# Kernel tuning notes

Measured on AMD Instinct MI355X. Metric: run time of the kernel, lower is better.

Reference implementation:

```python
import jax, jax.numpy as jnp
import numpy as np

TEMP = 0.1
EPS = 1e-12  # F.normalize eps


def setup_inputs() -> dict:
    key = jax.random.key(0)
    k1, k2 = jax.random.split(key)
    B, C, N = 8, 128, 4096
    features = jax.random.normal(k1, (B, C, N), dtype=jnp.float32)
    labels_all = jax.random.randint(k2, (B, N), 0, 16, dtype=jnp.int32)
    return {"features": features, "labels_all": labels_all}


def _per_cloud_loss(features_map, labels):
    # features_map: [C, N], labels: [N]
    v = features_map.T  # [N, C]
    v = v / jnp.maximum(jnp.linalg.norm(v, axis=1, keepdims=True), EPS)
    dp = jnp.exp(jnp.matmul(v, v.T) / TEMP)  # [N, N]
    n = dp.shape[0]
    # remove diagonal (dot_products - diag(diagonal))
    dp = dp * (1.0 - jnp.eye(n, dtype=dp.dtype))
    mask = labels[:, None] == labels[None, :]  # [N, N]
    positives = jnp.sum(jnp.where(mask, dp, 0.0), axis=1)
    negatives = jnp.sum(jnp.where(mask, 0.0, dp), axis=1)
    deviation = -jnp.log(positives / (positives + negatives))
    return jnp.mean(deviation)


def reference(features, labels_all):
    # features: [B, C, N], labels_all: [B, N]
    losses = jax.vmap(_per_cloud_loss)(features, labels_all)  # [B]
    return jnp.mean(losses)
```

## Files before the change

### kernel.cpp

```cpp
#include <hip/hip_runtime.h>
#include <hip/hip_bf16.h>
#include <math.h>

#define BATCH 8
#define NPTS 4096
#define CH 128
#define CTG 8
#define ROWS 128
#define CHUNK 32
#define NCHUNK (NPTS / (CTG * CHUNK))
#define NBUF 3

#define SQRT_TEMP_LOG2E 3.79828256f

typedef __attribute__((ext_vector_type(4))) float    f32x4;
typedef __attribute__((ext_vector_type(4))) int      i32x4;
typedef __attribute__((ext_vector_type(8))) short    bf16x8;
typedef __attribute__((ext_vector_type(4))) _Float16 f16x4;

typedef __attribute__((address_space(3))) unsigned int lds_uint;
typedef __attribute__((address_space(1))) const unsigned int gbl_uint;

__device__ __forceinline__ void load_lds16(const void* g, const void* l) {
    __builtin_amdgcn_global_load_lds((gbl_uint*)g, (lds_uint*)l, 16, 0, 0);
}

__device__ __forceinline__ float fast_exp2(float x) {
    return __builtin_amdgcn_exp2f(x);
}

__device__ __forceinline__ f32x4 mfma16(f16x4 a, f16x4 b, f32x4 c) {
#if __has_builtin(__builtin_amdgcn_mfma_f32_16x16x16f16)
    return __builtin_amdgcn_mfma_f32_16x16x16f16(a, b, c, 0, 0, 0);
#else
    f32x4 d = c;
    asm volatile("v_mfma_f32_16x16x16_f16 %0, %1, %2, %0"
                 : "+v"(d) : "v"(a), "v"(b));
    return d;
#endif
}

__global__ __launch_bounds__(256) void normalize_kernel(
    const float* __restrict__ f, __hip_bfloat16* __restrict__ vn,
    float* __restrict__ pos, float* __restrict__ neg, float* __restrict__ out)
{
    int idx = blockIdx.x * 256 + threadIdx.x;
    int point = idx >> 3, q = idx & 7;
    int b = point >> 12, n = point & (NPTS - 1);
    const float* base = f + (size_t)b * CH * NPTS + (size_t)(q * 16) * NPTS + n;

    float x[16];
    float ss = 0.0f;
    #pragma unroll
    for (int c = 0; c < 16; c++) {
        x[c] = base[(size_t)c * NPTS];
        ss += x[c] * x[c];
    }
    ss += __shfl_xor(ss, 1);
    ss += __shfl_xor(ss, 2);
    ss += __shfl_xor(ss, 4);
    float scale = SQRT_TEMP_LOG2E / fmaxf(sqrtf(ss), 1e-12f);

    __hip_bfloat16* outp = vn + (size_t)point * CH + q * 16;
    #pragma unroll
    for (int c0 = 0; c0 < 16; c0 += 8) {
        union { __hip_bfloat16 h[8]; uint4 u; } pk;
        #pragma unroll
        for (int j = 0; j < 8; j++)
            pk.h[j] = __float2bfloat16(x[c0 + j] * scale);
        *((uint4*)(outp + c0)) = pk.u;
    }
    if (q == 0) pos[point] = 0.0f;
    else if (q == 1) neg[point] = 0.0f;
    if (idx == 0) out[0] = 0.0f;
}

__global__ __launch_bounds__(256, 4) void tile_kernel(
    const __hip_bfloat16* __restrict__ vn, const int* __restrict__ labels,
    float* __restrict__ pos, float* __restrict__ neg)
{
    __shared__ short lB[NBUF][CHUNK * CH];
    __shared__ int labL[NPTS / CTG];

    const int ctg = blockIdx.x, rt = blockIdx.y, b = blockIdx.z;
    const int tid = threadIdx.x;
    const int w = tid >> 6, lane = tid & 63;
    const int lane15 = lane & 15, quad = lane >> 4;

    const int row0 = rt * ROWS;
    const int colbase = ctg * (NPTS / CTG);
    const __hip_bfloat16* vb = vn + (size_t)b * NPTS * CH;
    const int* labb = labels + b * NPTS;

    auto stage = [&](int buf, int chunk) {
        const __hip_bfloat16* Bb = vb + (size_t)(colbase + chunk * CHUNK) * CH;
        #pragma unroll
        for (int i = 0; i < 2; i++) {
            int ldsrow = w * 8 + i * 4;
            int r = ldsrow + quad;
            int g = lane15 ^ (r & 15);
            load_lds16(Bb + (size_t)r * CH + g * 8, &lB[buf][ldsrow * CH]);
        }
    };

    load_lds16(labb + colbase + (w & 1) * 256 + lane * 4, &labL[(w & 1) * 256]);

    bf16x8 afrag[2][4];
    int lr[2];
    #pragma unroll
    for (int mi = 0; mi < 2; mi++) {
        const int row_l = w * 32 + mi * 16 + lane15;
        const __hip_bfloat16* Arow = vb + (size_t)(row0 + row_l) * CH;
        #pragma unroll
        for (int ks = 0; ks < 4; ks++)
            afrag[mi][ks] = *(const bf16x8*)(Arow + (ks * 4 + quad) * 8);
        lr[mi] = labb[row0 + row_l];
    }

    stage(0, 0);
    stage(1, 1);

    int vad[2][4];
    #pragma unroll
    for (int ni = 0; ni < 2; ni++)
        #pragma unroll
        for (int ks = 0; ks < 4; ks++)
            vad[ni][ks] = (((ni * 16 + lane15) * CH) +
                           (((ks * 4 + quad) ^ lane15) << 3)) * 2;

    f32x4 qout[2] = {{0.0f, 0.0f, 0.0f, 0.0f}, {0.0f, 0.0f, 0.0f, 0.0f}};
    float ddiag[2] = {0.0f, 0.0f};
    const f32x4 zf = {0.0f, 0.0f, 0.0f, 0.0f};
    f32x4 accA[2][2], accB[2][2];

#define MFMA_PH(BUF_, ACC_)                                                   \
    {                                                                         \
        _Pragma("unroll")                                                     \
        for (int ni = 0; ni < 2; ni++) {                                      \
            bf16x8 bf = *(const bf16x8*)((const char*)(&lB[0][0]) +           \
                         (BUF_) * (CHUNK * CH * 2) + vad[ni][0]);             \
            ACC_[0][ni] = __builtin_amdgcn_mfma_f32_16x16x32_bf16(            \
                bf, afrag[0][0], zf, 0, 0, 0);                                \
            ACC_[1][ni] = __builtin_amdgcn_mfma_f32_16x16x32_bf16(            \
                bf, afrag[1][0], zf, 0, 0, 0);                                \
        }                                                                     \
        _Pragma("unroll")                                                     \
        for (int ks = 1; ks < 4; ks++) {                                      \
            _Pragma("unroll")                                                 \
            for (int ni = 0; ni < 2; ni++) {                                  \
                bf16x8 bf = *(const bf16x8*)((const char*)(&lB[0][0]) +       \
                             (BUF_) * (CHUNK * CH * 2) + vad[ni][ks]);        \
                ACC_[0][ni] = __builtin_amdgcn_mfma_f32_16x16x32_bf16(        \
                    bf, afrag[0][ks], ACC_[0][ni], 0, 0, 0);                  \
                ACC_[1][ni] = __builtin_amdgcn_mfma_f32_16x16x32_bf16(        \
                    bf, afrag[1][ks], ACC_[1][ni], 0, 0, 0);                  \
            }                                                                 \
        }                                                                     \
    }

#define EPI_PH(EC_, ACC_)                                                     \
    {                                                                         \
        _Pragma("unroll")                                                     \
        for (int ni = 0; ni < 2; ni++) {                                      \
            const i32x4 lc = *(const i32x4*)&labL[(EC_) * CHUNK + ni * 16 +   \
                                                  quad * 4];                  \
            f16x4 oh;                                                         \
            _Pragma("unroll")                                                 \
            for (int j = 0; j < 4; j++)                                       \
                oh[j] = (lc[j] == lane15) ? (_Float16)1.0f : (_Float16)0.0f;  \
            const int colblk = colbase + (EC_) * CHUNK + ni * 16;             \
            _Pragma("unroll")                                                 \
            for (int mi = 0; mi < 2; mi++) {                                  \
                f16x4 eh;                                                     \
                _Pragma("unroll")                                             \
                for (int r = 0; r < 4; r++)                                   \
                    eh[r] = (_Float16)fast_exp2(ACC_[mi][ni][r]);             \
                if (colblk == row0 + w * 32 + mi * 16) {    \
                    _Pragma("unroll")                                         \
                    for (int r = 0; r < 4; r++)                               \
                        if (lane15 == quad * 4 + r)                           \
                            ddiag[mi] += (float)eh[r];                        \
                }                                                             \
                qout[mi] = mfma16(oh, eh, qout[mi]);                          \
            }                                                                 \
        }                                                                     \
    }

#define BODY(C_, BUF_, CUR_, PRV_, DOEPI_)                                    \
    {                                                                         \
        __builtin_amdgcn_s_barrier();                                         \
        __builtin_amdgcn_s_setprio(1);                                        \
        MFMA_PH(BUF_, CUR_);                                                  \
        __builtin_amdgcn_s_setprio(0);                                        \
        stage(((BUF_) + 2) % 3, ((C_) + 2) & (NCHUNK - 1));                   \
        if (DOEPI_) { EPI_PH((C_) - 1, PRV_); }                               \
        asm volatile("s_waitcnt vmcnt(2)" ::: "memory");                      \
    }

    asm volatile("s_waitcnt vmcnt(2)" ::: "memory");
    BODY(0, 0, accA, accB, 0);
    #pragma unroll 1
    for (int c = 1; c <= 7; c += 6) {
        BODY(c + 0, 1, accB, accA, 1);
        BODY(c + 1, 2, accA, accB, 1);
        BODY(c + 2, 0, accB, accA, 1);
        BODY(c + 3, 1, accA, accB, 1);
        BODY(c + 4, 2, accB, accA, 1);
        BODY(c + 5, 0, accA, accB, 1);
    }
    BODY(13, 1, accB, accA, 1);
    BODY(14, 2, accA, accB, 1);
    __builtin_amdgcn_s_barrier();
    __builtin_amdgcn_s_setprio(1);
    MFMA_PH(0, accB);
    __builtin_amdgcn_s_setprio(0);
    EPI_PH(14, accA);
    EPI_PH(15, accB);

#undef BODY
#undef EPI_PH
#undef MFMA_PH

    #pragma unroll
    for (int mi = 0; mi < 2; mi++) {
        float p = -ddiag[mi], tt = -ddiag[mi];
        #pragma unroll
        for (int r = 0; r < 4; r++) {
            float v = qout[mi][r];
            tt += v;
            p  += (quad * 4 + r == lr[mi]) ? v : 0.0f;
        }
        p  += __shfl_xor(p, 16);   p  += __shfl_xor(p, 32);
        tt += __shfl_xor(tt, 16);  tt += __shfl_xor(tt, 32);
        if (lane < 16) {
            const int row_l = w * 32 + mi * 16 + lane15;
            atomicAdd(&pos[b * NPTS + row0 + row_l], p);
            atomicAdd(&neg[b * NPTS + row0 + row_l], tt - p);
        }
    }
}

__global__ __launch_bounds__(256) void finalize_kernel(
    const float* __restrict__ pos, const float* __restrict__ neg,
    float* __restrict__ out)
{
    int base = blockIdx.x * 1024 + threadIdx.x;
    float acc = 0.0f;
    #pragma unroll
    for (int k = 0; k < 4; k++) {
        int i = base + k * 256;
        float p = pos[i];
        float t = p + neg[i];
        acc += __logf(t / p);
    }
    #pragma unroll
    for (int off = 32; off; off >>= 1) acc += __shfl_down(acc, off);
    __shared__ float red[4];
    if ((threadIdx.x & 63) == 0) red[threadIdx.x >> 6] = acc;
    __syncthreads();
    if (threadIdx.x == 0) {
        float v = red[0] + red[1] + red[2] + red[3];
        atomicAdd(out, v * (1.0f / (BATCH * NPTS)));
    }
}

extern "C" void kernel_launch(void* const* d_in, const int* in_sizes, int n_in,
                              void* d_out, int out_size, void* d_ws, size_t ws_size,
                              hipStream_t stream)
{
    const float* features = (const float*)d_in[0];
    const int*   labels   = (const int*)d_in[1];
    float*       out      = (float*)d_out;

    __hip_bfloat16* vn = (__hip_bfloat16*)d_ws;
    float* pos = (float*)((char*)d_ws + (size_t)BATCH * NPTS * CH * sizeof(__hip_bfloat16));
    float* neg = pos + BATCH * NPTS;

    hipLaunchKernelGGL(normalize_kernel, dim3(BATCH * NPTS * 8 / 256), dim3(256), 0, stream,
                       features, vn, pos, neg, out);
    hipLaunchKernelGGL(tile_kernel, dim3(CTG, NPTS / ROWS, BATCH), dim3(256), 0, stream,
                       vn, labels, pos, neg);
    hipLaunchKernelGGL(finalize_kernel, dim3(32), dim3(256), 0, stream, pos, neg, out);
}
```

Before: 111.0 us.

## Deepen tile pipeline to six buffers and stage normalize output through LDS

The tile kernel now keeps six LDS buffers and handles chunks in pairs. It issues two stage loads per phase and interleaves the two MFMA phases with the exp epilogues, so more global loads stay in flight behind the compute. The normalize kernel is restructured so that each block handles 64 points across four channel groups. It reduces the norms through LDS and writes the bf16 output through a swizzled LDS staging buffer, giving coalesced 16-byte stores. The cost is double LDS use in the tile kernel, which may lower occupancy, and the normalize kernel now reads its input twice.

Result: no change. 113.2 us (+1.9%).

```diff
diff --git a/kernel.cpp b/kernel.cpp
--- a/kernel.cpp
+++ b/kernel.cpp
@@ -9,7 +9,7 @@
 #define ROWS 128
 #define CHUNK 32
 #define NCHUNK (NPTS / (CTG * CHUNK))
-#define NBUF 3
+#define NBUF 6
 
 #define SQRT_TEMP_LOG2E 3.79828256f
 
@@ -44,35 +44,60 @@
     const float* __restrict__ f, __hip_bfloat16* __restrict__ vn,
     float* __restrict__ pos, float* __restrict__ neg, float* __restrict__ out)
 {
-    int idx = blockIdx.x * 256 + threadIdx.x;
-    int point = idx >> 3, q = idx & 7;
-    int b = point >> 12, n = point & (NPTS - 1);
-    const float* base = f + (size_t)b * CH * NPTS + (size_t)(q * 16) * NPTS + n;
-
-    float x[16];
+    const int blk = blockIdx.x;
+    const int b = blk >> 6;
+    const int n0 = (blk & 63) * 64;
+    const int nl = threadIdx.x & 63;
+    const int cg = threadIdx.x >> 6;
+    const float* base = f + (size_t)b * CH * NPTS + (size_t)(cg * 32) * NPTS
+                          + n0 + nl;
+
+    __shared__ float red[4][64];
+    __shared__ float scl[64];
+    __shared__ short ostage[64 * CH];
+
     float ss = 0.0f;
     #pragma unroll
-    for (int c = 0; c < 16; c++) {
-        x[c] = base[(size_t)c * NPTS];
-        ss += x[c] * x[c];
-    }
-    ss += __shfl_xor(ss, 1);
-    ss += __shfl_xor(ss, 2);
-    ss += __shfl_xor(ss, 4);
-    float scale = SQRT_TEMP_LOG2E / fmaxf(sqrtf(ss), 1e-12f);
-
-    __hip_bfloat16* outp = vn + (size_t)point * CH + q * 16;
-    #pragma unroll
-    for (int c0 = 0; c0 < 16; c0 += 8) {
+    for (int c = 0; c < 32; c++) {
+        float v = base[(size_t)c * NPTS];
+        ss += v * v;
+    }
+    red[cg][nl] = ss;
+    __syncthreads();
+    if (cg == 0) {
+        float s = red[0][nl] + red[1][nl] + red[2][nl] + red[3][nl];
+        scl[nl] = SQRT_TEMP_LOG2E / fmaxf(sqrtf(s), 1e-12f);
+    }
+    __syncthreads();
+    const float scale = scl[nl];
+
+    #pragma unroll
+    for (int k = 0; k < 4; k++) {
         union { __hip_bfloat16 h[8]; uint4 u; } pk;
         #pragma unroll
-        for (int j = 0; j < 8; j++)
-            pk.h[j] = __float2bfloat16(x[c0 + j] * scale);
-        *((uint4*)(outp + c0)) = pk.u;
-    }
-    if (q == 0) pos[point] = 0.0f;
-    else if (q == 1) neg[point] = 0.0f;
-    if (idx == 0) out[0] = 0.0f;
+        for (int j = 0; j < 8; j++) {
+            float v = base[(size_t)(k * 8 + j) * NPTS] * scale;
+            pk.h[j] = __float2bfloat16(v);
+        }
+        const int ch8 = cg * 4 + k;
+        const int phys = (nl << 4) | (ch8 ^ (nl & 15));
+        *(uint4*)&ostage[phys * 8] = pk.u;
+    }
+    __syncthreads();
+
+    __hip_bfloat16* ob = vn + ((size_t)b * NPTS + n0) * CH;
+    const int t = threadIdx.x;
+    #pragma unroll
+    for (int it = 0; it < 4; it++) {
+        const int L = it * 256 + t;
+        const int pt = L >> 4, c8 = L & 15;
+        const int phys = (pt << 4) | (c8 ^ (pt & 15));
+        *(uint4*)(ob + (size_t)L * 8) = *(const uint4*)&ostage[phys * 8];
+    }
+
+    if (cg == 0) pos[b * NPTS + n0 + nl] = 0.0f;
+    else if (cg == 1) neg[b * NPTS + n0 + nl] = 0.0f;
+    if (blk == 0 && t == 0) out[0] = 0.0f;
 }
 
 __global__ __launch_bounds__(256, 4) void tile_kernel(
@@ -119,6 +144,8 @@
 
     stage(0, 0);
     stage(1, 1);
+    stage(2, 2);
+    stage(3, 3);
 
     int vad[2][4];
     #pragma unroll
@@ -186,38 +213,34 @@
         }                                                                     \
     }
 
-#define BODY(C_, BUF_, CUR_, PRV_, DOEPI_)                                    \
+#define PBODY(P_, BA_, BB_, DOEPI_)                                           \
     {                                                                         \
         __builtin_amdgcn_s_barrier();                                         \
         __builtin_amdgcn_s_setprio(1);                                        \
-        MFMA_PH(BUF_, CUR_);                                                  \
+        MFMA_PH(BA_, accA);                                                   \
         __builtin_amdgcn_s_setprio(0);                                        \
-        stage(((BUF_) + 2) % 3, ((C_) + 2) & (NCHUNK - 1));                   \
-        if (DOEPI_) { EPI_PH((C_) - 1, PRV_); }                               \
-        asm volatile("s_waitcnt vmcnt(2)" ::: "memory");                      \
-    }
-
-    asm volatile("s_waitcnt vmcnt(2)" ::: "memory");
-    BODY(0, 0, accA, accB, 0);
+        if (DOEPI_) { EPI_PH(2 * (P_) - 1, accB); }                           \
+        __builtin_amdgcn_s_setprio(1);                                        \
+        MFMA_PH(BB_, accB);                                                   \
+        __builtin_amdgcn_s_setprio(0);                                        \
+        stage(((BA_) + 4) % 6, (2 * (P_) + 4) & (NCHUNK - 1));                \
+        stage(((BB_) + 4) % 6, (2 * (P_) + 5) & (NCHUNK - 1));                \
+        EPI_PH(2 * (P_), accA);                                               \
+        asm volatile("s_waitcnt vmcnt(4)" ::: "memory");                      \
+    }
+
+    asm volatile("s_waitcnt vmcnt(4)" ::: "memory");
+    PBODY(0, 0, 1, 0);
     #pragma unroll 1
-    for (int c = 1; c <= 7; c += 6) {
-        BODY(c + 0, 1, accB, accA, 1);
-        BODY(c + 1, 2, accA, accB, 1);
-        BODY(c + 2, 0, accB, accA, 1);
-        BODY(c + 3, 1, accA, accB, 1);
-        BODY(c + 4, 2, accB, accA, 1);
-        BODY(c + 5, 0, accA, accB, 1);
-    }
-    BODY(13, 1, accB, accA, 1);
-    BODY(14, 2, accA, accB, 1);
-    __builtin_amdgcn_s_barrier();
-    __builtin_amdgcn_s_setprio(1);
-    MFMA_PH(0, accB);
-    __builtin_amdgcn_s_setprio(0);
-    EPI_PH(14, accA);
+    for (int p = 1; p <= 4; p += 3) {
+        PBODY(p + 0, 2, 3, 1);
+        PBODY(p + 1, 4, 5, 1);
+        PBODY(p + 2, 0, 1, 1);
+    }
+    PBODY(7, 2, 3, 1);
     EPI_PH(15, accB);
 
-#undef BODY
+#undef PBODY
 #undef EPI_PH
 #undef MFMA_PH
 
@@ -276,7 +299,7 @@
     float* pos = (float*)((char*)d_ws + (size_t)BATCH * NPTS * CH * sizeof(__hip_bfloat16));
     float* neg = pos + BATCH * NPTS;
 
-    hipLaunchKernelGGL(normalize_kernel, dim3(BATCH * NPTS * 8 / 256), dim3(256), 0, stream,
+    hipLaunchKernelGGL(normalize_kernel, dim3(512), dim3(256), 0, stream,
                        features, vn, pos, neg, out);
     hipLaunchKernelGGL(tile_kernel, dim3(CTG, NPTS / ROWS, BATCH), dim3(256), 0, stream,
                        vn, labels, pos, neg);
```
